# Performance work log

Measured on AMD Instinct MI355X. Metric: run time of the kernel, lower is better.

The kernel has to match this reference:

```python
import jax, jax.numpy as jnp
import numpy as np

HIDDEN = 128
N_NODES = 50000
N_EDGES = 640000


def setup_inputs() -> dict:
    key = jax.random.key(0)
    k1, k2, k3, k4, k5, k6, k7 = jax.random.split(key, 7)
    z = jax.random.normal(k1, (N_NODES, HIDDEN), dtype=jnp.float32)
    edge_index = jax.random.randint(k2, (2, N_EDGES), 0, N_NODES, dtype=jnp.int64)
    # Linear params (torch default uniform(-1/sqrt(fan_in), 1/sqrt(fan_in)))
    b1 = 1.0 / np.sqrt(2 * HIDDEN)
    W1 = jax.random.uniform(k3, (HIDDEN, 2 * HIDDEN), jnp.float32, -b1, b1)
    bias1 = jax.random.uniform(k4, (HIDDEN,), jnp.float32, -b1, b1)
    b2 = 1.0 / np.sqrt(HIDDEN)
    W2 = jax.random.uniform(k5, (1, HIDDEN), jnp.float32, -b2, b2)
    bias2 = jax.random.uniform(k6, (1,), jnp.float32, -b2, b2)
    return {"z": z, "W1": W1, "bias1": bias1, "W2": W2, "bias2": bias2,
            "edge_index": edge_index}


def reference(z, W1, bias1, W2, bias2, edge_index):
    # Gather endpoint embeddings: [E, H] each
    z_src = z[edge_index[0]]
    z_dst = z[edge_index[1]]
    h = jnp.concatenate([z_src, z_dst], axis=-1)  # [E, 2H]
    h = jax.nn.relu(h @ W1.T + bias1)             # [E, H]
    out = h @ W2.T + bias2                        # [E, 1]
    return out.reshape(-1)
```

## Files before the change

kernel.cpp:

```cpp
#include <hip/hip_runtime.h>
#include <hip/hip_bf16.h>


#define N_NODES 50000
#define N_EDGES 640000
#define H 128

using bf16 = __hip_bfloat16;
typedef __attribute__((ext_vector_type(8))) short short8;
typedef __attribute__((ext_vector_type(4))) float f32x4;
typedef __attribute__((ext_vector_type(2))) _Float16 h2v;

#define GLD_LDS16(g, l)                                                     \
  __builtin_amdgcn_global_load_lds(                                         \
      (const __attribute__((address_space(1))) void*)(g),                   \
      (__attribute__((address_space(3))) void*)(l), 16, 0, 0)

static __device__ __forceinline__ short bfbits(float x) {
  __hip_bfloat16 h = __float2bfloat16(x);
  return *reinterpret_cast<short*>(&h);
}

static __device__ __forceinline__ unsigned short h16(float x) {
  union { _Float16 h; unsigned short u; } c;
  c.h = (_Float16)x;
  return c.u;
}

static __device__ __forceinline__ h2v h2(unsigned u) {
  union { unsigned u; h2v h; } c; c.u = u; return c.h;
}

static __device__ __forceinline__ short8 pack8(float4 a, float4 b) {
  short8 r;
  r[0] = bfbits(a.x); r[1] = bfbits(a.y); r[2] = bfbits(a.z); r[3] = bfbits(a.w);
  r[4] = bfbits(b.x); r[5] = bfbits(b.y); r[6] = bfbits(b.z); r[7] = bfbits(b.w);
  return r;
}

__global__ __launch_bounds__(256) void w_to_bf16(const float* __restrict__ W1,
                                                 bf16* __restrict__ Wb) {
  const int u = blockIdx.x * 256 + threadIdx.x;
  const int o = u >> 4, k8 = (u & 15) * 8;
  const float4* src = reinterpret_cast<const float4*>(
      W1 + (size_t)(o & (H - 1)) * (2 * H) + (o >> 7) * H + k8);
  *reinterpret_cast<short8*>(Wb + (size_t)o * H + k8) = pack8(src[0], src[1]);
}

#define HP 136

__global__ __launch_bounds__(256) void precompute_uv(
    const float* __restrict__ z, const bf16* __restrict__ Wb,
    const float* __restrict__ bias1,
    _Float16* __restrict__ U, _Float16* __restrict__ V) {
  __shared__ float ldsF[32 * H];
  __shared__ bf16 ldsH[32 * HP];
  const int tid = threadIdx.x;
  const int lane = tid & 63;
  const int s = tid >> 6;
  const int l15 = lane & 15, quad = lane >> 4;
  const int nodebase = blockIdx.x * 32;

  {
    int r0 = nodebase + s * 8;
    if (r0 > N_NODES - 8) r0 = N_NODES - 8;
    const float* gsrc = z + (size_t)r0 * H + lane * 4;
    float* ldst = ldsF + s * 8 * H;
#pragma unroll
    for (int j = 0; j < 4; ++j) GLD_LDS16(gsrc + j * 256, ldst + j * 256);
  }

  short8 wf[4][4];
#pragma unroll
  for (int t = 0; t < 4; ++t) {
    const bf16* wp = Wb + (size_t)(s * 64 + t * 16 + l15) * H + quad * 8;
#pragma unroll
    for (int q = 0; q < 4; ++q)
      wf[t][q] = *reinterpret_cast<const short8*>(wp + q * 32);
  }

  __syncthreads();

  {
    const int row = tid >> 3, off = (tid & 7) * 16;
    const float4* fp = reinterpret_cast<const float4*>(ldsF + row * H + off);
    const float4 a = fp[0], b = fp[1], c = fp[2], d = fp[3];
    *reinterpret_cast<short8*>(&ldsH[row * HP + off]) = pack8(a, b);
    *reinterpret_cast<short8*>(&ldsH[row * HP + off + 8]) = pack8(c, d);
  }
  __syncthreads();

  short8 zf[2][4];
#pragma unroll
  for (int m = 0; m < 2; ++m)
#pragma unroll
    for (int q = 0; q < 4; ++q)
      zf[m][q] = *reinterpret_cast<const short8*>(
          &ldsH[(m * 16 + l15) * HP + quad * 8 + q * 32]);

  f32x4 acc[2][4] = {};
#pragma unroll
  for (int m = 0; m < 2; ++m)
#pragma unroll
    for (int t = 0; t < 4; ++t)
#pragma unroll
      for (int q = 0; q < 4; ++q)
        acc[m][t] =
            __builtin_amdgcn_mfma_f32_16x16x32_bf16(wf[t][q], zf[m][q], acc[m][t], 0, 0, 0);

  float4 b1v[4];
#pragma unroll
  for (int t = 0; t < 4; ++t)
    b1v[t] = (s < 2)
                 ? *reinterpret_cast<const float4*>(bias1 + s * 64 + t * 16 + quad * 4)
                 : make_float4(0.f, 0.f, 0.f, 0.f);

  _Float16* epi = reinterpret_cast<_Float16*>(ldsF);
#pragma unroll
  for (int m = 0; m < 2; ++m) {
    const int nl = m * 16 + l15;
#pragma unroll
    for (int t = 0; t < 4; ++t) {
      const int o = s * 64 + t * 16 + quad * 4;
      ushort4 st;
      st.x = h16(acc[m][t][0] + b1v[t].x);
      st.y = h16(acc[m][t][1] + b1v[t].y);
      st.z = h16(acc[m][t][2] + b1v[t].z);
      st.w = h16(acc[m][t][3] + b1v[t].w);
      *reinterpret_cast<ushort4*>(epi + nl * 256 + o) = st;
    }
  }
  __syncthreads();

#pragma unroll
  for (int half = 0; half < 2; ++half) {
    _Float16* base = half ? V : U;
#pragma unroll
    for (int it = 0; it < 2; ++it) {
      const int nl = s * 8 + it * 4 + (lane >> 4);
      const int oc = (lane & 15) * 8;
      const short8 v = *reinterpret_cast<const short8*>(epi + nl * 256 + half * H + oc);
      const int n = nodebase + nl;
      if (n < N_NODES)
        *reinterpret_cast<short8*>(base + (size_t)n * H + oc) = v;
    }
  }
}

static __device__ __forceinline__ h2v relu_fma(unsigned u, unsigned v,
                                               h2v w2, h2v acc) {
  const h2v h = __builtin_elementwise_max(h2(u) + h2(v), (h2v)(_Float16)0);
  return __builtin_elementwise_fma(h, w2, acc);
}

__global__ __launch_bounds__(256, 4) void edge_decode(
    const int* __restrict__ eidx, const _Float16* __restrict__ Ub,
    const _Float16* __restrict__ Vb, const float* __restrict__ W2,
    const float* __restrict__ bias2, float* __restrict__ out) {
  const int lane = threadIdx.x & 63;
  const int w = blockIdx.x * 4 + (int)(threadIdx.x >> 6);
  const int chunk = w * 64;
  const int e8 = lane & 7;

  h2v w2h[8];
  const float4* wp = reinterpret_cast<const float4*>(W2 + e8 * 16);
#pragma unroll
  for (int q = 0; q < 4; ++q) {
    const float4 wv = wp[q];
    w2h[2 * q][0] = (_Float16)wv.x; w2h[2 * q][1] = (_Float16)wv.y;
    w2h[2 * q + 1][0] = (_Float16)wv.z; w2h[2 * q + 1][1] = (_Float16)wv.w;
  }
  const float b2 = bias2[0];

  const int src = eidx[chunk + lane];
  const int dst = eidx[N_EDGES + chunk + lane];
  const uint4* U4 = reinterpret_cast<const uint4*>(Ub);
  const uint4* V4 = reinterpret_cast<const uint4*>(Vb);

  float res = 0.f;
#pragma unroll
  for (int hb = 0; hb < 2; ++hb) {
    uint4 ua[4], ub[4], va[4], vb[4];
#pragma unroll
    for (int j = 0; j < 4; ++j) {
      const int i = hb * 4 + j;
      const int sl = (lane & 56) + i;
      const int s_i = __shfl(src, sl);
      const int d_i = __shfl(dst, sl);
      const uint4* up = U4 + (size_t)s_i * 16 + e8 * 2;
      const uint4* vp = V4 + (size_t)d_i * 16 + e8 * 2;
      ua[j] = up[0]; ub[j] = up[1];
      va[j] = vp[0]; vb[j] = vp[1];
    }
#pragma unroll
    for (int j = 0; j < 4; ++j) {
      const int i = hb * 4 + j;
      h2v acc = (h2v)(_Float16)0;
      acc = relu_fma(ua[j].x, va[j].x, w2h[0], acc);
      acc = relu_fma(ua[j].y, va[j].y, w2h[1], acc);
      acc = relu_fma(ua[j].z, va[j].z, w2h[2], acc);
      acc = relu_fma(ua[j].w, va[j].w, w2h[3], acc);
      acc = relu_fma(ub[j].x, vb[j].x, w2h[4], acc);
      acc = relu_fma(ub[j].y, vb[j].y, w2h[5], acc);
      acc = relu_fma(ub[j].z, vb[j].z, w2h[6], acc);
      acc = relu_fma(ub[j].w, vb[j].w, w2h[7], acc);
      float sum = (float)acc[0] + (float)acc[1];
      sum += __shfl_xor(sum, 1);
      sum += __shfl_xor(sum, 2);
      sum += __shfl_xor(sum, 4);
      if (e8 == i) res = sum + b2;
    }
  }
  out[chunk + lane] = res;
}

extern "C" void kernel_launch(void* const* d_in, const int* in_sizes, int n_in,
                              void* d_out, int out_size, void* d_ws, size_t ws_size,
                              hipStream_t stream) {
  const float* z     = (const float*)d_in[0];
  const float* W1    = (const float*)d_in[1];
  const float* bias1 = (const float*)d_in[2];
  const float* W2    = (const float*)d_in[3];
  const float* bias2 = (const float*)d_in[4];
  const int*   eidx  = (const int*)d_in[5];
  float* out = (float*)d_out;

  _Float16* U  = (_Float16*)d_ws;
  _Float16* V  = U + (size_t)N_NODES * H;
  bf16*     Wb = (bf16*)(V + (size_t)N_NODES * H);

  hipLaunchKernelGGL(w_to_bf16, dim3(16), dim3(256), 0, stream, W1, Wb);
  hipLaunchKernelGGL(precompute_uv, dim3((N_NODES + 31) / 32), dim3(256), 0, stream,
                     z, Wb, bias1, U, V);
  hipLaunchKernelGGL(edge_decode, dim3(N_EDGES / 64 / 4), dim3(256), 0, stream,
                     eidx, U, V, W2, bias2, out);
}
```

Baseline: 138.8 us.

## Bucket-sort edges by source node to improve gather locality in edge decode

```diff
diff --git a/kernel.cpp b/kernel.cpp
--- a/kernel.cpp
+++ b/kernel.cpp
@@ -5,6 +5,9 @@
 #define N_NODES 50000
 #define N_EDGES 640000
 #define H 128
+#define NBUCKETS 196
+#define NCHUNKS (N_EDGES / 64)
+#define CPX (NCHUNKS / 8)
 
 using bf16 = __hip_bfloat16;
 typedef __attribute__((ext_vector_type(8))) short short8;
@@ -147,6 +150,47 @@
   }
 }
 
+__global__ __launch_bounds__(256) void edge_hist(const int* __restrict__ eidx,
+                                                 int* __restrict__ ghist) {
+  __shared__ int h[NBUCKETS];
+  const int t = threadIdx.x;
+  if (t < NBUCKETS) h[t] = 0;
+  __syncthreads();
+  const int e = blockIdx.x * 256 + t;
+  atomicAdd(&h[eidx[e] >> 8], 1);
+  __syncthreads();
+  if (t < NBUCKETS) atomicAdd(&ghist[t], h[t]);
+}
+
+__global__ __launch_bounds__(256) void bucket_scan(const int* __restrict__ ghist,
+                                                   int* __restrict__ cursor) {
+  __shared__ int s[256];
+  const int t = threadIdx.x;
+  const int v = (t < NBUCKETS) ? ghist[t] : 0;
+  s[t] = v;
+  __syncthreads();
+#pragma unroll
+  for (int off = 1; off < 256; off <<= 1) {
+    const int add = (t >= off) ? s[t - off] : 0;
+    __syncthreads();
+    s[t] += add;
+    __syncthreads();
+  }
+  if (t < NBUCKETS) cursor[t] = s[t] - v;
+}
+
+__global__ __launch_bounds__(256) void edge_scatter(const int* __restrict__ eidx,
+                                                    int* __restrict__ cursor,
+                                                    unsigned* __restrict__ ssd,
+                                                    int* __restrict__ seid) {
+  const int e = blockIdx.x * 256 + threadIdx.x;
+  const int s = eidx[e];
+  const int d = eidx[N_EDGES + e];
+  const int p = atomicAdd(&cursor[s >> 8], 1);
+  ssd[p] = ((unsigned)s << 16) | (unsigned)d;
+  seid[p] = e;
+}
+
 static __device__ __forceinline__ h2v relu_fma(unsigned u, unsigned v,
                                                h2v w2, h2v acc) {
   const h2v h = __builtin_elementwise_max(h2(u) + h2(v), (h2v)(_Float16)0);
@@ -154,12 +198,15 @@
 }
 
 __global__ __launch_bounds__(256, 4) void edge_decode(
-    const int* __restrict__ eidx, const _Float16* __restrict__ Ub,
-    const _Float16* __restrict__ Vb, const float* __restrict__ W2,
-    const float* __restrict__ bias2, float* __restrict__ out) {
+    const unsigned* __restrict__ ssd, const int* __restrict__ seid,
+    const _Float16* __restrict__ Ub, const _Float16* __restrict__ Vb,
+    const float* __restrict__ W2, const float* __restrict__ bias2,
+    float* __restrict__ out) {
   const int lane = threadIdx.x & 63;
-  const int w = blockIdx.x * 4 + (int)(threadIdx.x >> 6);
-  const int chunk = w * 64;
+  const int x = blockIdx.x & 7;
+  const int lc = (blockIdx.x >> 3) * 4 + (int)(threadIdx.x >> 6);
+  if (lc >= CPX) return;
+  const int chunk = (x * CPX + lc) * 64;
   const int e8 = lane & 7;
 
   h2v w2h[8];
@@ -172,8 +219,8 @@
   }
   const float b2 = bias2[0];
 
-  const int src = eidx[chunk + lane];
-  const int dst = eidx[N_EDGES + chunk + lane];
+  const int sd = (int)ssd[chunk + lane];
+  const int eid = seid[chunk + lane];
   const uint4* U4 = reinterpret_cast<const uint4*>(Ub);
   const uint4* V4 = reinterpret_cast<const uint4*>(Vb);
 
@@ -184,9 +231,9 @@
 #pragma unroll
     for (int j = 0; j < 4; ++j) {
       const int i = hb * 4 + j;
-      const int sl = (lane & 56) + i;
-      const int s_i = __shfl(src, sl);
-      const int d_i = __shfl(dst, sl);
+      const int sdb = __shfl(sd, (lane & 56) + i);
+      const int s_i = ((unsigned)sdb) >> 16;
+      const int d_i = sdb & 0xffff;
       const uint4* up = U4 + (size_t)s_i * 16 + e8 * 2;
       const uint4* vp = V4 + (size_t)d_i * 16 + e8 * 2;
       ua[j] = up[0]; ub[j] = up[1];
@@ -211,7 +258,7 @@
       if (e8 == i) res = sum + b2;
     }
   }
-  out[chunk + lane] = res;
+  out[eid] = res;
 }
 
 extern "C" void kernel_launch(void* const* d_in, const int* in_sizes, int n_in,
@@ -225,13 +272,23 @@
   const int*   eidx  = (const int*)d_in[5];
   float* out = (float*)d_out;
 
-  _Float16* U  = (_Float16*)d_ws;
-  _Float16* V  = U + (size_t)N_NODES * H;
-  bf16*     Wb = (bf16*)(V + (size_t)N_NODES * H);
-
+  _Float16* U    = (_Float16*)d_ws;
+  _Float16* V    = U + (size_t)N_NODES * H;
+  bf16*     Wb   = (bf16*)(V + (size_t)N_NODES * H);
+  unsigned* ssd  = (unsigned*)(Wb + 256 * H);
+  int*      seid = (int*)(ssd + N_EDGES);
+  int*      ghist = seid + N_EDGES;
+  int*      cursor = ghist + 256;
+
+  hipMemsetAsync(ghist, 0, 512 * sizeof(int), stream);
   hipLaunchKernelGGL(w_to_bf16, dim3(16), dim3(256), 0, stream, W1, Wb);
   hipLaunchKernelGGL(precompute_uv, dim3((N_NODES + 31) / 32), dim3(256), 0, stream,
                      z, Wb, bias1, U, V);
-  hipLaunchKernelGGL(edge_decode, dim3(N_EDGES / 64 / 4), dim3(256), 0, stream,
-                     eidx, U, V, W2, bias2, out);
-}
+  hipLaunchKernelGGL(edge_hist, dim3(N_EDGES / 256), dim3(256), 0, stream,
+                     eidx, ghist);
+  hipLaunchKernelGGL(bucket_scan, dim3(1), dim3(256), 0, stream, ghist, cursor);
+  hipLaunchKernelGGL(edge_scatter, dim3(N_EDGES / 256), dim3(256), 0, stream,
+                     eidx, cursor, ssd, seid);
+  hipLaunchKernelGGL(edge_decode, dim3(2504), dim3(256), 0, stream,
+                     ssd, seid, U, V, W2, bias2, out);
+}
```

Result: slower. 540.9 us (+289.7%).

## Fuse W1 bf16 conversion into persistent precompute_uv kernel

Applied to the files above, without the earlier changes.

```diff
diff --git a/kernel.cpp b/kernel.cpp
--- a/kernel.cpp
+++ b/kernel.cpp
@@ -5,6 +5,9 @@
 #define N_NODES 50000
 #define N_EDGES 640000
 #define H 128
+#define NTILES ((N_NODES + 31) / 32)
+#define GRIDA 782
+#define HP 136
 
 using bf16 = __hip_bfloat16;
 typedef __attribute__((ext_vector_type(8))) short short8;
@@ -38,19 +41,14 @@
   return r;
 }
 
-__global__ __launch_bounds__(256) void w_to_bf16(const float* __restrict__ W1,
-                                                 bf16* __restrict__ Wb) {
-  const int u = blockIdx.x * 256 + threadIdx.x;
-  const int o = u >> 4, k8 = (u & 15) * 8;
-  const float4* src = reinterpret_cast<const float4*>(
-      W1 + (size_t)(o & (H - 1)) * (2 * H) + (o >> 7) * H + k8);
-  *reinterpret_cast<short8*>(Wb + (size_t)o * H + k8) = pack8(src[0], src[1]);
-}
-
-#define HP 136
+static __device__ __forceinline__ h2v relu_fma(unsigned u, unsigned v,
+                                               h2v w2, h2v acc) {
+  const h2v h = __builtin_elementwise_max(h2(u) + h2(v), (h2v)(_Float16)0);
+  return __builtin_elementwise_fma(h, w2, acc);
+}
 
 __global__ __launch_bounds__(256) void precompute_uv(
-    const float* __restrict__ z, const bf16* __restrict__ Wb,
+    const float* __restrict__ z, const float* __restrict__ W1,
     const float* __restrict__ bias1,
     _Float16* __restrict__ U, _Float16* __restrict__ V) {
   __shared__ float ldsF[32 * H];
@@ -59,54 +57,18 @@
   const int lane = tid & 63;
   const int s = tid >> 6;
   const int l15 = lane & 15, quad = lane >> 4;
-  const int nodebase = blockIdx.x * 32;
-
-  {
-    int r0 = nodebase + s * 8;
-    if (r0 > N_NODES - 8) r0 = N_NODES - 8;
-    const float* gsrc = z + (size_t)r0 * H + lane * 4;
-    float* ldst = ldsF + s * 8 * H;
-#pragma unroll
-    for (int j = 0; j < 4; ++j) GLD_LDS16(gsrc + j * 256, ldst + j * 256);
-  }
 
   short8 wf[4][4];
 #pragma unroll
   for (int t = 0; t < 4; ++t) {
-    const bf16* wp = Wb + (size_t)(s * 64 + t * 16 + l15) * H + quad * 8;
-#pragma unroll
-    for (int q = 0; q < 4; ++q)
-      wf[t][q] = *reinterpret_cast<const short8*>(wp + q * 32);
-  }
-
-  __syncthreads();
-
-  {
-    const int row = tid >> 3, off = (tid & 7) * 16;
-    const float4* fp = reinterpret_cast<const float4*>(ldsF + row * H + off);
-    const float4 a = fp[0], b = fp[1], c = fp[2], d = fp[3];
-    *reinterpret_cast<short8*>(&ldsH[row * HP + off]) = pack8(a, b);
-    *reinterpret_cast<short8*>(&ldsH[row * HP + off + 8]) = pack8(c, d);
-  }
-  __syncthreads();
-
-  short8 zf[2][4];
-#pragma unroll
-  for (int m = 0; m < 2; ++m)
-#pragma unroll
-    for (int q = 0; q < 4; ++q)
-      zf[m][q] = *reinterpret_cast<const short8*>(
-          &ldsH[(m * 16 + l15) * HP + quad * 8 + q * 32]);
-
-  f32x4 acc[2][4] = {};
-#pragma unroll
-  for (int m = 0; m < 2; ++m)
-#pragma unroll
-    for (int t = 0; t < 4; ++t)
-#pragma unroll
-      for (int q = 0; q < 4; ++q)
-        acc[m][t] =
-            __builtin_amdgcn_mfma_f32_16x16x32_bf16(wf[t][q], zf[m][q], acc[m][t], 0, 0, 0);
+    const int o = s * 64 + t * 16 + l15;
+    const float* wp = W1 + (size_t)(o & (H - 1)) * (2 * H) + (o >> 7) * H + quad * 8;
+#pragma unroll
+    for (int q = 0; q < 4; ++q) {
+      const float4* p = reinterpret_cast<const float4*>(wp + q * 32);
+      wf[t][q] = pack8(p[0], p[1]);
+    }
+  }
 
   float4 b1v[4];
 #pragma unroll
@@ -115,42 +77,78 @@
                  ? *reinterpret_cast<const float4*>(bias1 + s * 64 + t * 16 + quad * 4)
                  : make_float4(0.f, 0.f, 0.f, 0.f);
 
-  _Float16* epi = reinterpret_cast<_Float16*>(ldsF);
-#pragma unroll
-  for (int m = 0; m < 2; ++m) {
-    const int nl = m * 16 + l15;
-#pragma unroll
-    for (int t = 0; t < 4; ++t) {
-      const int o = s * 64 + t * 16 + quad * 4;
-      ushort4 st;
-      st.x = h16(acc[m][t][0] + b1v[t].x);
-      st.y = h16(acc[m][t][1] + b1v[t].y);
-      st.z = h16(acc[m][t][2] + b1v[t].z);
-      st.w = h16(acc[m][t][3] + b1v[t].w);
-      *reinterpret_cast<ushort4*>(epi + nl * 256 + o) = st;
-    }
-  }
-  __syncthreads();
-
-#pragma unroll
-  for (int half = 0; half < 2; ++half) {
-    _Float16* base = half ? V : U;
-#pragma unroll
-    for (int it = 0; it < 2; ++it) {
-      const int nl = s * 8 + it * 4 + (lane >> 4);
-      const int oc = (lane & 15) * 8;
-      const short8 v = *reinterpret_cast<const short8*>(epi + nl * 256 + half * H + oc);
-      const int n = nodebase + nl;
-      if (n < N_NODES)
-        *reinterpret_cast<short8*>(base + (size_t)n * H + oc) = v;
-    }
-  }
-}
-
-static __device__ __forceinline__ h2v relu_fma(unsigned u, unsigned v,
-                                               h2v w2, h2v acc) {
-  const h2v h = __builtin_elementwise_max(h2(u) + h2(v), (h2v)(_Float16)0);
-  return __builtin_elementwise_fma(h, w2, acc);
+  for (int tile = blockIdx.x; tile < NTILES; tile += GRIDA) {
+    const int nodebase = tile * 32;
+
+    {
+      int r0 = nodebase + s * 8;
+      if (r0 > N_NODES - 8) r0 = N_NODES - 8;
+      const float* gsrc = z + (size_t)r0 * H + lane * 4;
+      float* ldst = ldsF + s * 8 * H;
+#pragma unroll
+      for (int j = 0; j < 4; ++j) GLD_LDS16(gsrc + j * 256, ldst + j * 256);
+    }
+    __syncthreads();
+
+    {
+      const int row = tid >> 3, off = (tid & 7) * 16;
+      const float4* fp = reinterpret_cast<const float4*>(ldsF + row * H + off);
+      const float4 a = fp[0], b = fp[1], c = fp[2], d = fp[3];
+      *reinterpret_cast<short8*>(&ldsH[row * HP + off]) = pack8(a, b);
+      *reinterpret_cast<short8*>(&ldsH[row * HP + off + 8]) = pack8(c, d);
+    }
+    __syncthreads();
+
+    short8 zf[2][4];
+#pragma unroll
+    for (int m = 0; m < 2; ++m)
+#pragma unroll
+      for (int q = 0; q < 4; ++q)
+        zf[m][q] = *reinterpret_cast<const short8*>(
+            &ldsH[(m * 16 + l15) * HP + quad * 8 + q * 32]);
+
+    f32x4 acc[2][4] = {};
+#pragma unroll
+    for (int m = 0; m < 2; ++m)
+#pragma unroll
+      for (int t = 0; t < 4; ++t)
+#pragma unroll
+        for (int q = 0; q < 4; ++q)
+          acc[m][t] = __builtin_amdgcn_mfma_f32_16x16x32_bf16(wf[t][q], zf[m][q],
+                                                              acc[m][t], 0, 0, 0);
+
+    _Float16* epi = reinterpret_cast<_Float16*>(ldsF);
+#pragma unroll
+    for (int m = 0; m < 2; ++m) {
+      const int nl = m * 16 + l15;
+#pragma unroll
+      for (int t = 0; t < 4; ++t) {
+        const int o = s * 64 + t * 16 + quad * 4;
+        ushort4 st;
+        st.x = h16(acc[m][t][0] + b1v[t].x);
+        st.y = h16(acc[m][t][1] + b1v[t].y);
+        st.z = h16(acc[m][t][2] + b1v[t].z);
+        st.w = h16(acc[m][t][3] + b1v[t].w);
+        *reinterpret_cast<ushort4*>(epi + nl * 256 + o) = st;
+      }
+    }
+    __syncthreads();
+
+#pragma unroll
+    for (int half = 0; half < 2; ++half) {
+      _Float16* base = half ? V : U;
+#pragma unroll
+      for (int it = 0; it < 2; ++it) {
+        const int nl = s * 8 + it * 4 + (lane >> 4);
+        const int oc = (lane & 15) * 8;
+        const short8 v = *reinterpret_cast<const short8*>(epi + nl * 256 + half * H + oc);
+        const int n = nodebase + nl;
+        if (n < N_NODES)
+          *reinterpret_cast<short8*>(base + (size_t)n * H + oc) = v;
+      }
+    }
+    __syncthreads();
+  }
 }
 
 __global__ __launch_bounds__(256, 4) void edge_decode(
@@ -225,13 +223,11 @@
   const int*   eidx  = (const int*)d_in[5];
   float* out = (float*)d_out;
 
-  _Float16* U  = (_Float16*)d_ws;
-  _Float16* V  = U + (size_t)N_NODES * H;
-  bf16*     Wb = (bf16*)(V + (size_t)N_NODES * H);
-
-  hipLaunchKernelGGL(w_to_bf16, dim3(16), dim3(256), 0, stream, W1, Wb);
-  hipLaunchKernelGGL(precompute_uv, dim3((N_NODES + 31) / 32), dim3(256), 0, stream,
-                     z, Wb, bias1, U, V);
+  _Float16* U = (_Float16*)d_ws;
+  _Float16* V = U + (size_t)N_NODES * H;
+
+  hipLaunchKernelGGL(precompute_uv, dim3(GRIDA), dim3(256), 0, stream,
+                     z, W1, bias1, U, V);
   hipLaunchKernelGGL(edge_decode, dim3(N_EDGES / 64 / 4), dim3(256), 0, stream,
                      eidx, U, V, W2, bias2, out);
 }
```

Measured after the change: 146.3 us. +5.4%, slower.
